# Optimization experiments

Measured on AMD Instinct MI355X. Metric: run time of the kernel, lower is better.

Reference implementation:

```python
import jax, jax.numpy as jnp
import numpy as np

N, C, E, H = 50000, 128, 1_600_000, 32
JITTER = 1e-20


def _lin(k, fan_in, fan_out):
    return jax.random.normal(k, (fan_in, fan_out), jnp.float32) / np.sqrt(fan_in)


def setup_inputs() -> dict:
    key = jax.random.key(0)
    ks = jax.random.split(key, 20)
    x = jax.random.normal(ks[0], (N, C), jnp.float32)
    edge_index = jax.random.randint(ks[1], (2, E), 0, N, dtype=jnp.int64)
    inp = {"x": x, "edge_index": edge_index}
    # actor params
    inp["aW"] = _lin(ks[2], C, C); inp["ab"] = jnp.zeros((C,), jnp.float32)
    inp["a1W"] = _lin(ks[3], C, H); inp["a1b"] = jnp.zeros((H,), jnp.float32)
    inp["a2W"] = _lin(ks[4], H, H); inp["a2b"] = jnp.zeros((H,), jnp.float32)
    inp["a3W"] = _lin(ks[5], H, 2); inp["a3b"] = jnp.zeros((2,), jnp.float32)
    # critic params
    inp["cW"] = _lin(ks[6], C, C); inp["cb"] = jnp.zeros((C,), jnp.float32)
    inp["c1W"] = _lin(ks[7], C, H); inp["c1b"] = jnp.zeros((H,), jnp.float32)
    inp["c2W"] = _lin(ks[8], H, H); inp["c2b"] = jnp.zeros((H,), jnp.float32)
    inp["c3W"] = _lin(ks[9], H, 2); inp["c3b"] = jnp.zeros((2,), jnp.float32)
    return inp


def gcn_conv(x, src, dst, W, b):
    """Standard PyG GCNConv: add self-loops, symmetric degree norm, X@W, scatter-add, +bias."""
    n = x.shape[0]
    loop = jnp.arange(n)
    s = jnp.concatenate([src, loop])  # [E+N]
    d = jnp.concatenate([dst, loop])
    deg = jax.ops.segment_sum(jnp.ones_like(d, jnp.float32), d, num_segments=n)
    dinv = jnp.where(deg > 0, jax.lax.rsqrt(deg), 0.0)
    norm = dinv[s] * dinv[d]                     # [E+N]
    h = x @ W                                    # [N, C]
    agg = jax.ops.segment_sum(h[s] * norm[:, None], d, num_segments=n)
    return agg + b


def reference(x, edge_index, aW, ab, a1W, a1b, a2W, a2b, a3W, a3b,
              cW, cb, c1W, c1b, c2W, c2b, c3W, c3b):
    src, dst = edge_index[0], edge_index[1]
    # actor
    h = jax.nn.relu(gcn_conv(x, src, dst, aW, ab)) + x
    h = jax.nn.relu(h @ a1W + a1b)
    h = jax.nn.relu(h @ a2W + a2b)
    a = h @ a3W + a3b                            # [N, 2]
    concentration = jax.nn.softplus(a[:, 0]) + JITTER
    p = jax.nn.softplus(a[:, 1])
    action2_probs = p / jnp.sum(p)
    # critic
    hc = jax.nn.relu(gcn_conv(x, src, dst, cW, cb)) + x
    hc = jnp.sum(hc, axis=0)                     # [C]
    hc = jax.nn.relu(hc @ c1W + c1b)
    hc = jax.nn.relu(hc @ c2W + c2b)
    value = hc @ c3W + c3b                       # [2]
    return (concentration, value, action2_probs)
```

## Files before the change

kernel.cpp:

```cpp
#include <hip/hip_runtime.h>
#include <hip/hip_bf16.h>
#include <hip/hip_fp16.h>
#include <math.h>

#define C 128
#define BCAP 12288

using half8x = __attribute__((ext_vector_type(8))) _Float16;
using half4x = __attribute__((ext_vector_type(4))) _Float16;
using f32x4  = __attribute__((ext_vector_type(4))) float;

__device__ inline float4 h4_to_f4(uint2 u) {
    __half2 p0 = *(__half2*)&u.x;
    __half2 p1 = *(__half2*)&u.y;
    float2 f0 = __half22float2(p0), f1 = __half22float2(p1);
    return make_float4(f0.x, f0.y, f1.x, f1.y);
}

__device__ inline float softplusf(float v) {
    return (v > 20.f) ? v : log1pf(expf(v));
}

__global__ __launch_bounds__(256) void initk(unsigned* gcur, float* colsum, float* pSum) {
    int t = threadIdx.x;
    gcur[t] = 0u;
    if (t < 128) colsum[t] = 0.f;
    if (t == 128) pSum[0] = 0.f;
}

__global__ __launch_bounds__(256) void wtk(const float* __restrict__ aW, const float* __restrict__ cW,
                                           const float* __restrict__ a1W,
                                           __half* __restrict__ wt, __half* __restrict__ a1wt) {
    int idx = blockIdx.x * 256 + threadIdx.x;
    if (idx < 32768) {
        int y = idx >> 14, r = idx & 16383;
        int k = r >> 7, n = r & 127;
        const float* W = y ? cW : aW;
        wt[((size_t)y << 14) + n * 128 + k] = __float2half(W[k * 128 + n]);
    } else if (idx < 36864) {
        int r = idx - 32768;
        int k = r >> 5, n = r & 31;
        a1wt[n * 128 + k] = __float2half(a1W[k * 32 + n]);
    }
}

__global__ __launch_bounds__(256) void bink(const int* __restrict__ ei,
                                            unsigned* __restrict__ gcur,
                                            unsigned* __restrict__ gstage,
                                            int E, int NBKT) {
    __shared__ unsigned raw[6400];
    __shared__ unsigned image[6400];
    __shared__ unsigned cnt[256];
    __shared__ unsigned pref[256];
    __shared__ unsigned cur[256];
    __shared__ unsigned gb[256];
    int t = threadIdx.x, b = blockIdx.x;
    int elo = (int)((long long)b * E / 256);
    int ehi = (int)((long long)(b + 1) * E / 256);
    int n = ehi - elo;

    for (int i = t; i < n; i += 256) {
        int d = __builtin_nontemporal_load(ei + E + elo + i);
        int s = __builtin_nontemporal_load(ei + elo + i);
        raw[i] = (unsigned)s | ((unsigned)(d & 255) << 16) | ((unsigned)(d >> 8) << 24);
    }
    cnt[t] = 0u; cur[t] = 0u;
    __syncthreads();
    for (int i = t; i < n; i += 256) atomicAdd(&cnt[raw[i] >> 24], 1u);
    __syncthreads();
    pref[t] = cnt[t];
    __syncthreads();
    for (int off = 1; off < 256; off <<= 1) {
        unsigned add = (t >= off) ? pref[t - off] : 0u;
        __syncthreads();
        pref[t] += add;
        __syncthreads();
    }
    gb[t] = (t < NBKT && cnt[t]) ? atomicAdd(&gcur[t], cnt[t]) : 0u;
    __syncthreads();
    for (int i = t; i < n; i += 256) {
        unsigned v = raw[i];
        unsigned B = v >> 24;
        unsigned pos = (pref[B] - cnt[B]) + atomicAdd(&cur[B], 1u);
        image[pos] = v & 0xFFFFFFu;
    }
    __syncthreads();
    int wv = t >> 6, lane = t & 63;
    for (int B = wv; B < NBKT; B += 4) {
        unsigned c = cnt[B];
        if (!c) continue;
        unsigned eb = pref[B] - c;
        unsigned gbase = gb[B];
        unsigned c2 = (gbase < BCAP) ? ((c < BCAP - gbase) ? c : BCAP - gbase) : 0u;
        for (unsigned i = lane; i < c2; i += 64)
            gstage[(size_t)B * BCAP + gbase + i] = image[eb + i];
    }
}

__global__ void bktscank(const unsigned* __restrict__ gcur, unsigned* __restrict__ bktbase, int NBKT) {
    __shared__ unsigned tmp[256];
    int t = threadIdx.x;
    unsigned g = (t < NBKT) ? gcur[t] : 0u;
    unsigned v = (g < BCAP) ? g : BCAP;
    tmp[t] = v;
    __syncthreads();
    for (int off = 1; off < 256; off <<= 1) {
        unsigned add = (t >= off) ? tmp[t - off] : 0u;
        __syncthreads();
        tmp[t] += add;
        __syncthreads();
    }
    if (t < NBKT) bktbase[t] = tmp[t] - v;
}

__global__ __launch_bounds__(256) void placek(const unsigned* __restrict__ gstage,
                                              const unsigned* __restrict__ gcur,
                                              const unsigned* __restrict__ bktbase,
                                              int* __restrict__ rowptr, float* __restrict__ dinv,
                                              int* __restrict__ col, int N, int NBKT) {
    __shared__ unsigned image[BCAP];
    __shared__ unsigned cnt[256];
    __shared__ unsigned pref[256];
    __shared__ unsigned cur[256];
    int B = blockIdx.x, t = threadIdx.x;
    unsigned g = gcur[B];
    unsigned m = (g < BCAP) ? g : BCAP;
    unsigned base = bktbase[B];
    const unsigned* st = gstage + (size_t)B * BCAP;

    cnt[t] = 0u; cur[t] = 0u;
    __syncthreads();
    for (unsigned i = t; i < m; i += 256) atomicAdd(&cnt[(st[i] >> 16) & 255u], 1u);
    __syncthreads();
    pref[t] = cnt[t];
    __syncthreads();
    for (int off = 1; off < 256; off <<= 1) {
        unsigned add = (t >= off) ? pref[t - off] : 0u;
        __syncthreads();
        pref[t] += add;
        __syncthreads();
    }
    int d = B * 256 + t;
    if (d < N) {
        rowptr[d] = (int)(base + pref[t] - cnt[t]);
        dinv[d] = rsqrtf((float)(cnt[t] + 1u));
    }
    if (B == NBKT - 1 && t == 0) rowptr[N] = (int)(base + m);
    for (unsigned i = t; i < m; i += 256) {
        unsigned v = st[i];
        unsigned dl = (v >> 16) & 255u;
        unsigned pos = (pref[dl] - cnt[dl]) + atomicAdd(&cur[dl], 1u);
        image[pos] = v & 0xFFFFu;
    }
    __syncthreads();
    for (unsigned i = t; i < m; i += 256) col[base + i] = (int)image[i];
}

__global__ __launch_bounds__(256) void xhk(const float* __restrict__ x, const float* __restrict__ dinv,
                                           __half* __restrict__ xh, __half* __restrict__ x16, int N) {
    int i = blockIdx.x * 256 + threadIdx.x;
    if (i >= N * 64) return;
    int node = i >> 6, fp = (i & 63) * 2;
    float w = dinv[node];
    float2 f = *(const float2*)&x[(size_t)node * C + fp];
    __half2 h = __floats2half2_rn(f.x * w, f.y * w);
    __half2 hx = __floats2half2_rn(f.x, f.y);
    *(unsigned*)&xh[(size_t)node * C + fp] = *(unsigned*)&h;
    *(unsigned*)&x16[(size_t)node * C + fp] = *(unsigned*)&hx;
}

__global__ __launch_bounds__(256) void gatherk(const int* __restrict__ col,
                                               const int* __restrict__ rowptr,
                                               const __half* __restrict__ xh,
                                               const float* __restrict__ dinv,
                                               __half* __restrict__ gg, int N) {
    __shared__ int snb[4][64];
    int t = threadIdx.x;
    int wid = t >> 6, lane = t & 63;
    int d = blockIdx.x * 4 + wid;
    if (d >= N) return;
    int beg = rowptr[d], end = rowptr[d + 1];
    int half = lane >> 5, sub = lane & 31;
    int f = sub * 4;

    float a0 = 0.f, a1 = 0.f, a2 = 0.f, a3 = 0.f;

    for (int c = beg; c < end; c += 64) {
        if (c + lane < end) snb[wid][lane] = col[c + lane];
        int n = end - c; if (n > 64) n = 64;
        int j = 0;
        for (; j + 3 < n; j += 4) {
            size_t i0 = (size_t)snb[wid][j + half] * C + f;
            size_t i1 = (size_t)snb[wid][j + 2 + half] * C + f;
            float4 v0 = h4_to_f4(*(const uint2*)&xh[i0]);
            float4 v1 = h4_to_f4(*(const uint2*)&xh[i1]);
            a0 += v0.x + v1.x;
            a1 += v0.y + v1.y;
            a2 += v0.z + v1.z;
            a3 += v0.w + v1.w;
        }
        for (; j < n; j += 2) {
            if (j + half < n) {
                float4 v = h4_to_f4(*(const uint2*)&xh[(size_t)snb[wid][j + half] * C + f]);
                a0 += v.x; a1 += v.y; a2 += v.z; a3 += v.w;
            }
        }
    }
    a0 += __shfl_xor(a0, 32, 64);
    a1 += __shfl_xor(a1, 32, 64);
    a2 += __shfl_xor(a2, 32, 64);
    a3 += __shfl_xor(a3, 32, 64);

    if (half == 0) {
        float4 s4 = h4_to_f4(*(const uint2*)&xh[(size_t)d * C + f]);
        float dv = dinv[d];
        __half2 h0 = __floats2half2_rn((a0 + s4.x) * dv, (a1 + s4.y) * dv);
        __half2 h1 = __floats2half2_rn((a2 + s4.z) * dv, (a3 + s4.w) * dv);
        uint2 u; u.x = *(unsigned*)&h0; u.y = *(unsigned*)&h1;
        *(uint2*)&gg[(size_t)d * C + f] = u;
    }
}

__global__ __launch_bounds__(256) void gemm2k(const __half* __restrict__ gg,
                                              const __half* __restrict__ wt,
                                              const __half* __restrict__ a1wt,
                                              const float* __restrict__ ab, const float* __restrict__ cb,
                                              const __half* __restrict__ x16,
                                              const float* __restrict__ a1b,
                                              const float* __restrict__ a2W, const float* __restrict__ a2b,
                                              const float* __restrict__ a3W, const float* __restrict__ a3b,
                                              float* __restrict__ scratch,
                                              float* __restrict__ out, float* __restrict__ pSum, int N) {
    __shared__ char As[16384];
    __shared__ char Aux[8192];
    const bool actor = (blockIdx.y == 0);
    const float* bias = actor ? ab : cb;
    const __half* W = wt + (actor ? 0 : 16384);
    const int row0 = blockIdx.x * 64;
    const int t = threadIdx.x;

    _Float16* w2t = (_Float16*)Aux;
    _Float16* h1b = (_Float16*)(Aux + 2560);
    float* w3s    = (float*)(Aux + 7680);
    float* scol   = (float*)Aux;

#pragma unroll
    for (int i = 0; i < 4; ++i) {
        int c = t + i * 256;
        int row = c >> 4, cb16 = (c & 15) * 16;
        int grow = row0 + row;
        uint4 u = make_uint4(0u, 0u, 0u, 0u);
        if (grow < N) u = *(const uint4*)&gg[(size_t)grow * C + (c & 15) * 8];
        *(uint4*)(As + row * 256 + (cb16 ^ ((row & 7) << 4))) = u;
    }
    if (actor) {
#pragma unroll
        for (int i = 0; i < 4; ++i) {
            int idx = t + i * 256;
            int k = idx >> 5, n = idx & 31;
            w2t[n * 40 + k] = (_Float16)a2W[idx];
        }
        if (t < 64) w3s[t] = a3W[t];
    }
    __syncthreads();

    int wv = t >> 6, l = t & 63;
    int lm = l & 15, lk = l >> 4;
    int koffB = lk * 16;
    int koffH = lk * 8;

    const int rowA = wv * 16 + lm;
    const int grow = row0 + rowA;
    const bool valid = grow < N;
    const int sw = (rowA & 7) << 4;

    half8x af[4];
    {
        const char* rp = As + rowA * 256;
#pragma unroll
        for (int kc = 0; kc < 4; ++kc)
            af[kc] = *(const half8x*)(rp + ((kc * 64 + koffB) ^ sw));
    }

#pragma unroll
    for (int nc = 0; nc < 8; ++nc) {
        const __half* wp = W + (nc * 16 + lm) * 128;
        half8x bf[4];
#pragma unroll
        for (int kc = 0; kc < 4; ++kc)
            bf[kc] = *(const half8x*)(wp + kc * 32 + koffH);
        f32x4 acc = {0.f, 0.f, 0.f, 0.f};
#pragma unroll
        for (int kc = 0; kc < 4; ++kc)
            acc = __builtin_amdgcn_mfma_f32_16x16x32_f16(bf[kc], af[kc], acc, 0, 0, 0);
        float4 bv = *(const float4*)&bias[nc * 16 + lk * 4];
        half4x xq = {};
        if (valid) xq = *(const half4x*)&x16[(size_t)grow * C + nc * 16 + lk * 4];
        float v0 = valid ? fmaxf(acc[0] + bv.x, 0.f) + (float)xq[0] : 0.f;
        float v1 = valid ? fmaxf(acc[1] + bv.y, 0.f) + (float)xq[1] : 0.f;
        float v2 = valid ? fmaxf(acc[2] + bv.z, 0.f) + (float)xq[2] : 0.f;
        float v3 = valid ? fmaxf(acc[3] + bv.w, 0.f) + (float)xq[3] : 0.f;
        if (actor) {
            half4x hv = { (_Float16)v0, (_Float16)v1, (_Float16)v2, (_Float16)v3 };
            *(half4x*)(As + rowA * 256 + ((nc * 32 + lk * 8) ^ sw)) = hv;
        } else {
            v0 += __shfl_xor(v0, 1, 64); v0 += __shfl_xor(v0, 2, 64);
            v0 += __shfl_xor(v0, 4, 64); v0 += __shfl_xor(v0, 8, 64);
            v1 += __shfl_xor(v1, 1, 64); v1 += __shfl_xor(v1, 2, 64);
            v1 += __shfl_xor(v1, 4, 64); v1 += __shfl_xor(v1, 8, 64);
            v2 += __shfl_xor(v2, 1, 64); v2 += __shfl_xor(v2, 2, 64);
            v2 += __shfl_xor(v2, 4, 64); v2 += __shfl_xor(v2, 8, 64);
            v3 += __shfl_xor(v3, 1, 64); v3 += __shfl_xor(v3, 2, 64);
            v3 += __shfl_xor(v3, 4, 64); v3 += __shfl_xor(v3, 8, 64);
            if (lm == 0) {
                float4 st = make_float4(v0, v1, v2, v3);
                *(float4*)&scol[wv * 128 + nc * 16 + lk * 4] = st;
            }
        }
    }
    __syncthreads();

    if (actor) {
        half8x a1f[4];
        {
            const char* rp = As + rowA * 256;
#pragma unroll
            for (int kc = 0; kc < 4; ++kc)
                a1f[kc] = *(const half8x*)(rp + ((kc * 64 + koffB) ^ sw));
        }
#pragma unroll
        for (int ct = 0; ct < 2; ++ct) {
            const __half* ap = a1wt + (ct * 16 + lm) * 128;
            f32x4 acc1 = {0.f, 0.f, 0.f, 0.f};
#pragma unroll
            for (int kc = 0; kc < 4; ++kc) {
                half8x bq = *(const half8x*)(ap + kc * 32 + koffH);
                acc1 = __builtin_amdgcn_mfma_f32_16x16x32_f16(bq, a1f[kc], acc1, 0, 0, 0);
            }
            float4 b1v = *(const float4*)&a1b[ct * 16 + lk * 4];
            half4x h = { (_Float16)fmaxf(acc1[0] + b1v.x, 0.f),
                         (_Float16)fmaxf(acc1[1] + b1v.y, 0.f),
                         (_Float16)fmaxf(acc1[2] + b1v.z, 0.f),
                         (_Float16)fmaxf(acc1[3] + b1v.w, 0.f) };
            *(half4x*)((char*)h1b + rowA * 80 + ct * 32 + lk * 8) = h;
        }

        half4x alo = *(const half4x*)((char*)h1b + rowA * 80 + lk * 16);
        half4x ahi = *(const half4x*)((char*)h1b + rowA * 80 + lk * 16 + 8);
        half8x a2f = __builtin_shufflevector(alo, ahi, 0, 1, 2, 3, 4, 5, 6, 7);
        float p0 = 0.f, p1 = 0.f;
#pragma unroll
        for (int ct = 0; ct < 2; ++ct) {
            half4x blo = *(const half4x*)((char*)w2t + (ct * 16 + lm) * 80 + lk * 16);
            half4x bhi = *(const half4x*)((char*)w2t + (ct * 16 + lm) * 80 + lk * 16 + 8);
            half8x b2f = __builtin_shufflevector(blo, bhi, 0, 1, 2, 3, 4, 5, 6, 7);
            f32x4 acc2 = {0.f, 0.f, 0.f, 0.f};
            acc2 = __builtin_amdgcn_mfma_f32_16x16x32_f16(b2f, a2f, acc2, 0, 0, 0);
            float4 b2v = *(const float4*)&a2b[ct * 16 + lk * 4];
#pragma unroll
            for (int j = 0; j < 4; ++j) {
                int f = ct * 16 + lk * 4 + j;
                float h2v = fmaxf(acc2[j] + (&b2v.x)[j], 0.f);
                float2 w3 = *(const float2*)&w3s[f * 2];
                p0 += h2v * w3.x;
                p1 += h2v * w3.y;
            }
        }
        p0 += __shfl_xor(p0, 16, 64); p0 += __shfl_xor(p0, 32, 64);
        p1 += __shfl_xor(p1, 16, 64); p1 += __shfl_xor(p1, 32, 64);
        float wave_psum = 0.f;
        if (lk == 0 && valid) {
            float s0 = softplusf(p0 + a3b[0]);
            float s1 = softplusf(p1 + a3b[1]);
            out[grow] = s0 + 1e-20f;
            out[(size_t)N + 2 + grow] = s1;
            wave_psum = s1;
        }
        wave_psum += __shfl_xor(wave_psum, 1, 64);
        wave_psum += __shfl_xor(wave_psum, 2, 64);
        wave_psum += __shfl_xor(wave_psum, 4, 64);
        wave_psum += __shfl_xor(wave_psum, 8, 64);
        wave_psum += __shfl_xor(wave_psum, 16, 64);
        wave_psum += __shfl_xor(wave_psum, 32, 64);
        if (l == 0) atomicAdd(pSum, wave_psum);
    } else {
        if (t < 128)
            scratch[(size_t)blockIdx.x * 128 + t] = scol[t] + scol[128 + t] + scol[256 + t] + scol[384 + t];
    }
}

__global__ __launch_bounds__(128) void csredk(const float* __restrict__ scratch, float* __restrict__ colsum, int nblk) {
    int t = threadIdx.x;
    float s = 0.f;
    for (int b = blockIdx.x; b < nblk; b += gridDim.x)
        s += scratch[(size_t)b * 128 + t];
    atomicAdd(&colsum[t], s);
}

__global__ void critick(const float* __restrict__ colsum,
                        const float* __restrict__ c1W, const float* __restrict__ c1b,
                        const float* __restrict__ c2W, const float* __restrict__ c2b,
                        const float* __restrict__ c3W, const float* __restrict__ c3b,
                        float* __restrict__ out, int N) {
    __shared__ float s1[32], s2[32];
    int t = threadIdx.x;
    if (t < 32) {
        float acc = c1b[t];
        for (int k = 0; k < 128; ++k) acc += colsum[k] * c1W[k * 32 + t];
        s1[t] = fmaxf(acc, 0.f);
    }
    __syncthreads();
    if (t < 32) {
        float acc = c2b[t];
        for (int k = 0; k < 32; ++k) acc += s1[k] * c2W[k * 32 + t];
        s2[t] = fmaxf(acc, 0.f);
    }
    __syncthreads();
    if (t < 2) {
        float acc = c3b[t];
        for (int k = 0; k < 32; ++k) acc += s2[k] * c3W[k * 2 + t];
        out[(size_t)N + t] = acc;
    }
}

__global__ __launch_bounds__(256) void normk(float* __restrict__ out, const float* __restrict__ pSum, int N) {
    int i = blockIdx.x * 256 + threadIdx.x;
    if (i < N) out[(size_t)N + 2 + i] /= pSum[0];
}

extern "C" void kernel_launch(void* const* d_in, const int* in_sizes, int n_in,
                              void* d_out, int out_size, void* d_ws, size_t ws_size,
                              hipStream_t stream) {
    const float* x   = (const float*)d_in[0];
    const int* ei    = (const int*)d_in[1];
    const float* aW  = (const float*)d_in[2];
    const float* ab  = (const float*)d_in[3];
    const float* a1W = (const float*)d_in[4];
    const float* a1b = (const float*)d_in[5];
    const float* a2W = (const float*)d_in[6];
    const float* a2b = (const float*)d_in[7];
    const float* a3W = (const float*)d_in[8];
    const float* a3b = (const float*)d_in[9];
    const float* cW  = (const float*)d_in[10];
    const float* cb  = (const float*)d_in[11];
    const float* c1W = (const float*)d_in[12];
    const float* c1b = (const float*)d_in[13];
    const float* c2W = (const float*)d_in[14];
    const float* c2b = (const float*)d_in[15];
    const float* c3W = (const float*)d_in[16];
    const float* c3b = (const float*)d_in[17];

    const int N = in_sizes[0] / C;
    const int E = in_sizes[1] / 2;
    const int NBKT = (N + 255) / 256;
    const int nblk64 = (N + 63) / 64;
    float* out = (float*)d_out;

    char* ws = (char*)d_ws;
    size_t off = 0;
    auto alloc = [&](size_t bytes) {
        size_t o = off;
        off = (off + bytes + 255) & ~(size_t)255;
        return (void*)(ws + o);
    };
    unsigned* gcur    = (unsigned*)alloc(256 * 4);
    unsigned* bktbase = (unsigned*)alloc(256 * 4);
    unsigned* gstage  = (unsigned*)alloc((size_t)NBKT * BCAP * 4);
    int* rowptr       = (int*)alloc((size_t)(N + 1) * 4);
    float* dinv       = (float*)alloc((size_t)N * 4);
    int* colidx       = (int*)alloc((size_t)E * 4);
    __half* xh        = (__half*)alloc((size_t)N * C * 2);
    __half* x16       = (__half*)alloc((size_t)N * C * 2);
    __half* gg        = (__half*)alloc((size_t)N * C * 2);
    __half* wt        = (__half*)alloc(2 * 16384 * 2);
    __half* a1wt      = (__half*)alloc(4096 * 2);
    float* scratch    = (float*)alloc((size_t)nblk64 * 128 * 4);
    float* colsum     = (float*)alloc(128 * 4);
    float* pSum       = (float*)alloc(4);

    initk<<<1, 256, 0, stream>>>(gcur, colsum, pSum);
    wtk<<<144, 256, 0, stream>>>(aW, cW, a1W, wt, a1wt);
    bink<<<256, 256, 0, stream>>>(ei, gcur, gstage, E, NBKT);
    bktscank<<<1, 256, 0, stream>>>(gcur, bktbase, NBKT);
    placek<<<NBKT, 256, 0, stream>>>(gstage, gcur, bktbase, rowptr, dinv, colidx, N, NBKT);
    xhk<<<(N * 64 + 255) / 256, 256, 0, stream>>>(x, dinv, xh, x16, N);
    gatherk<<<(N + 3) / 4, 256, 0, stream>>>(colidx, rowptr, xh, dinv, gg, N);
    gemm2k<<<dim3(nblk64, 2), 256, 0, stream>>>(gg, wt, a1wt, ab, cb, x16,
                                                a1b, a2W, a2b, a3W, a3b,
                                                scratch, out, pSum, N);
    csredk<<<8, 128, 0, stream>>>(scratch, colsum, nblk64);
    critick<<<1, 64, 0, stream>>>(colsum, c1W, c1b, c2W, c2b, c3W, c3b, out, N);
    normk<<<(N + 255) / 256, 256, 0, stream>>>(out, pSum, N);
}
```

Measured before the change: 236.5 us.

## Merge actor and critic GEMM blocks into one block sharing the A tile

Before, separate blocks handled the actor and the critic, and each one loaded the same 64-row aggregated feature tile and the same x16 residual. Now one block per row tile runs both 128x128 MFMA GEMMs from a single A-fragment load, then does the critic column reduction and the actor MLP head. Weight fragments for the next column chunk are prefetched into registers while the current one computes. This halves the gg and x16 reads and the block count, but raises register pressure (two accumulator and weight sets plus prefetch buffers) and LDS use, which may lower occupancy.

```diff
diff --git a/kernel.cpp b/kernel.cpp
--- a/kernel.cpp
+++ b/kernel.cpp
@@ -232,17 +232,14 @@
                                               float* __restrict__ scratch,
                                               float* __restrict__ out, float* __restrict__ pSum, int N) {
     __shared__ char As[16384];
-    __shared__ char Aux[8192];
-    const bool actor = (blockIdx.y == 0);
-    const float* bias = actor ? ab : cb;
-    const __half* W = wt + (actor ? 0 : 16384);
-    const int row0 = blockIdx.x * 64;
-    const int t = threadIdx.x;
-
+    __shared__ char Aux[10240];
     _Float16* w2t = (_Float16*)Aux;
     _Float16* h1b = (_Float16*)(Aux + 2560);
     float* w3s    = (float*)(Aux + 7680);
-    float* scol   = (float*)Aux;
+    float* scol   = (float*)(Aux + 7936);
+
+    const int row0 = blockIdx.x * 64;
+    const int t = threadIdx.x;
 
 #pragma unroll
     for (int i = 0; i < 4; ++i) {
@@ -253,15 +250,13 @@
         if (grow < N) u = *(const uint4*)&gg[(size_t)grow * C + (c & 15) * 8];
         *(uint4*)(As + row * 256 + (cb16 ^ ((row & 7) << 4))) = u;
     }
-    if (actor) {
-#pragma unroll
-        for (int i = 0; i < 4; ++i) {
-            int idx = t + i * 256;
-            int k = idx >> 5, n = idx & 31;
-            w2t[n * 40 + k] = (_Float16)a2W[idx];
-        }
-        if (t < 64) w3s[t] = a3W[t];
-    }
+#pragma unroll
+    for (int i = 0; i < 4; ++i) {
+        int idx = t + i * 256;
+        int k = idx >> 5, n = idx & 31;
+        w2t[n * 40 + k] = (_Float16)a2W[idx];
+    }
+    if (t < 64) w3s[t] = a3W[t];
     __syncthreads();
 
     int wv = t >> 6, l = t & 63;
@@ -282,28 +277,55 @@
             af[kc] = *(const half8x*)(rp + ((kc * 64 + koffB) ^ sw));
     }
 
+    const __half* WA = wt;
+    const __half* WC = wt + 16384;
+
+    half8x bfA[4], bfC[4];
+    {
+        const __half* wpA = WA + lm * 128;
+        const __half* wpC = WC + lm * 128;
+#pragma unroll
+        for (int kc = 0; kc < 4; ++kc) {
+            bfA[kc] = *(const half8x*)(wpA + kc * 32 + koffH);
+            bfC[kc] = *(const half8x*)(wpC + kc * 32 + koffH);
+        }
+    }
+
 #pragma unroll
     for (int nc = 0; nc < 8; ++nc) {
-        const __half* wp = W + (nc * 16 + lm) * 128;
-        half8x bf[4];
-#pragma unroll
-        for (int kc = 0; kc < 4; ++kc)
-            bf[kc] = *(const half8x*)(wp + kc * 32 + koffH);
-        f32x4 acc = {0.f, 0.f, 0.f, 0.f};
-#pragma unroll
-        for (int kc = 0; kc < 4; ++kc)
-            acc = __builtin_amdgcn_mfma_f32_16x16x32_f16(bf[kc], af[kc], acc, 0, 0, 0);
-        float4 bv = *(const float4*)&bias[nc * 16 + lk * 4];
+        half8x nA[4], nC[4];
+        if (nc < 7) {
+            const __half* wpA = WA + ((nc + 1) * 16 + lm) * 128;
+            const __half* wpC = WC + ((nc + 1) * 16 + lm) * 128;
+#pragma unroll
+            for (int kc = 0; kc < 4; ++kc) {
+                nA[kc] = *(const half8x*)(wpA + kc * 32 + koffH);
+                nC[kc] = *(const half8x*)(wpC + kc * 32 + koffH);
+            }
+        }
+        f32x4 accA = {0.f, 0.f, 0.f, 0.f};
+        f32x4 accC = {0.f, 0.f, 0.f, 0.f};
+#pragma unroll
+        for (int kc = 0; kc < 4; ++kc) {
+            accA = __builtin_amdgcn_mfma_f32_16x16x32_f16(bfA[kc], af[kc], accA, 0, 0, 0);
+            accC = __builtin_amdgcn_mfma_f32_16x16x32_f16(bfC[kc], af[kc], accC, 0, 0, 0);
+        }
+        float4 bvA = *(const float4*)&ab[nc * 16 + lk * 4];
+        float4 bvC = *(const float4*)&cb[nc * 16 + lk * 4];
         half4x xq = {};
         if (valid) xq = *(const half4x*)&x16[(size_t)grow * C + nc * 16 + lk * 4];
-        float v0 = valid ? fmaxf(acc[0] + bv.x, 0.f) + (float)xq[0] : 0.f;
-        float v1 = valid ? fmaxf(acc[1] + bv.y, 0.f) + (float)xq[1] : 0.f;
-        float v2 = valid ? fmaxf(acc[2] + bv.z, 0.f) + (float)xq[2] : 0.f;
-        float v3 = valid ? fmaxf(acc[3] + bv.w, 0.f) + (float)xq[3] : 0.f;
-        if (actor) {
-            half4x hv = { (_Float16)v0, (_Float16)v1, (_Float16)v2, (_Float16)v3 };
+        {
+            half4x hv = { (_Float16)(valid ? fmaxf(accA[0] + bvA.x, 0.f) + (float)xq[0] : 0.f),
+                          (_Float16)(valid ? fmaxf(accA[1] + bvA.y, 0.f) + (float)xq[1] : 0.f),
+                          (_Float16)(valid ? fmaxf(accA[2] + bvA.z, 0.f) + (float)xq[2] : 0.f),
+                          (_Float16)(valid ? fmaxf(accA[3] + bvA.w, 0.f) + (float)xq[3] : 0.f) };
             *(half4x*)(As + rowA * 256 + ((nc * 32 + lk * 8) ^ sw)) = hv;
-        } else {
+        }
+        {
+            float v0 = valid ? fmaxf(accC[0] + bvC.x, 0.f) + (float)xq[0] : 0.f;
+            float v1 = valid ? fmaxf(accC[1] + bvC.y, 0.f) + (float)xq[1] : 0.f;
+            float v2 = valid ? fmaxf(accC[2] + bvC.z, 0.f) + (float)xq[2] : 0.f;
+            float v3 = valid ? fmaxf(accC[3] + bvC.w, 0.f) + (float)xq[3] : 0.f;
             v0 += __shfl_xor(v0, 1, 64); v0 += __shfl_xor(v0, 2, 64);
             v0 += __shfl_xor(v0, 4, 64); v0 += __shfl_xor(v0, 8, 64);
             v1 += __shfl_xor(v1, 1, 64); v1 += __shfl_xor(v1, 2, 64);
@@ -312,81 +334,81 @@
             v2 += __shfl_xor(v2, 4, 64); v2 += __shfl_xor(v2, 8, 64);
             v3 += __shfl_xor(v3, 1, 64); v3 += __shfl_xor(v3, 2, 64);
             v3 += __shfl_xor(v3, 4, 64); v3 += __shfl_xor(v3, 8, 64);
-            if (lm == 0) {
-                float4 st = make_float4(v0, v1, v2, v3);
-                *(float4*)&scol[wv * 128 + nc * 16 + lk * 4] = st;
-            }
-        }
-    }
-    __syncthreads();
-
-    if (actor) {
-        half8x a1f[4];
-        {
-            const char* rp = As + rowA * 256;
-#pragma unroll
-            for (int kc = 0; kc < 4; ++kc)
-                a1f[kc] = *(const half8x*)(rp + ((kc * 64 + koffB) ^ sw));
-        }
-#pragma unroll
-        for (int ct = 0; ct < 2; ++ct) {
-            const __half* ap = a1wt + (ct * 16 + lm) * 128;
-            f32x4 acc1 = {0.f, 0.f, 0.f, 0.f};
-#pragma unroll
-            for (int kc = 0; kc < 4; ++kc) {
-                half8x bq = *(const half8x*)(ap + kc * 32 + koffH);
-                acc1 = __builtin_amdgcn_mfma_f32_16x16x32_f16(bq, a1f[kc], acc1, 0, 0, 0);
-            }
-            float4 b1v = *(const float4*)&a1b[ct * 16 + lk * 4];
-            half4x h = { (_Float16)fmaxf(acc1[0] + b1v.x, 0.f),
-                         (_Float16)fmaxf(acc1[1] + b1v.y, 0.f),
-                         (_Float16)fmaxf(acc1[2] + b1v.z, 0.f),
-                         (_Float16)fmaxf(acc1[3] + b1v.w, 0.f) };
-            *(half4x*)((char*)h1b + rowA * 80 + ct * 32 + lk * 8) = h;
-        }
-
-        half4x alo = *(const half4x*)((char*)h1b + rowA * 80 + lk * 16);
-        half4x ahi = *(const half4x*)((char*)h1b + rowA * 80 + lk * 16 + 8);
-        half8x a2f = __builtin_shufflevector(alo, ahi, 0, 1, 2, 3, 4, 5, 6, 7);
-        float p0 = 0.f, p1 = 0.f;
-#pragma unroll
-        for (int ct = 0; ct < 2; ++ct) {
-            half4x blo = *(const half4x*)((char*)w2t + (ct * 16 + lm) * 80 + lk * 16);
-            half4x bhi = *(const half4x*)((char*)w2t + (ct * 16 + lm) * 80 + lk * 16 + 8);
-            half8x b2f = __builtin_shufflevector(blo, bhi, 0, 1, 2, 3, 4, 5, 6, 7);
-            f32x4 acc2 = {0.f, 0.f, 0.f, 0.f};
-            acc2 = __builtin_amdgcn_mfma_f32_16x16x32_f16(b2f, a2f, acc2, 0, 0, 0);
-            float4 b2v = *(const float4*)&a2b[ct * 16 + lk * 4];
-#pragma unroll
-            for (int j = 0; j < 4; ++j) {
-                int f = ct * 16 + lk * 4 + j;
-                float h2v = fmaxf(acc2[j] + (&b2v.x)[j], 0.f);
-                float2 w3 = *(const float2*)&w3s[f * 2];
-                p0 += h2v * w3.x;
-                p1 += h2v * w3.y;
-            }
-        }
-        p0 += __shfl_xor(p0, 16, 64); p0 += __shfl_xor(p0, 32, 64);
-        p1 += __shfl_xor(p1, 16, 64); p1 += __shfl_xor(p1, 32, 64);
-        float wave_psum = 0.f;
-        if (lk == 0 && valid) {
-            float s0 = softplusf(p0 + a3b[0]);
-            float s1 = softplusf(p1 + a3b[1]);
-            out[grow] = s0 + 1e-20f;
-            out[(size_t)N + 2 + grow] = s1;
-            wave_psum = s1;
-        }
-        wave_psum += __shfl_xor(wave_psum, 1, 64);
-        wave_psum += __shfl_xor(wave_psum, 2, 64);
-        wave_psum += __shfl_xor(wave_psum, 4, 64);
-        wave_psum += __shfl_xor(wave_psum, 8, 64);
-        wave_psum += __shfl_xor(wave_psum, 16, 64);
-        wave_psum += __shfl_xor(wave_psum, 32, 64);
-        if (l == 0) atomicAdd(pSum, wave_psum);
-    } else {
-        if (t < 128)
-            scratch[(size_t)blockIdx.x * 128 + t] = scol[t] + scol[128 + t] + scol[256 + t] + scol[384 + t];
-    }
+            if (lm == 0)
+                *(float4*)&scol[wv * 128 + nc * 16 + lk * 4] = make_float4(v0, v1, v2, v3);
+        }
+        if (nc < 7) {
+#pragma unroll
+            for (int kc = 0; kc < 4; ++kc) { bfA[kc] = nA[kc]; bfC[kc] = nC[kc]; }
+        }
+    }
+    __syncthreads();
+
+    if (t < 128)
+        scratch[(size_t)blockIdx.x * 128 + t] = scol[t] + scol[128 + t] + scol[256 + t] + scol[384 + t];
+
+    half8x a1f[4];
+    {
+        const char* rp = As + rowA * 256;
+#pragma unroll
+        for (int kc = 0; kc < 4; ++kc)
+            a1f[kc] = *(const half8x*)(rp + ((kc * 64 + koffB) ^ sw));
+    }
+#pragma unroll
+    for (int ct = 0; ct < 2; ++ct) {
+        const __half* ap = a1wt + (ct * 16 + lm) * 128;
+        f32x4 acc1 = {0.f, 0.f, 0.f, 0.f};
+#pragma unroll
+        for (int kc = 0; kc < 4; ++kc) {
+            half8x bq = *(const half8x*)(ap + kc * 32 + koffH);
+            acc1 = __builtin_amdgcn_mfma_f32_16x16x32_f16(bq, a1f[kc], acc1, 0, 0, 0);
+        }
+        float4 b1v = *(const float4*)&a1b[ct * 16 + lk * 4];
+        half4x h = { (_Float16)fmaxf(acc1[0] + b1v.x, 0.f),
+                     (_Float16)fmaxf(acc1[1] + b1v.y, 0.f),
+                     (_Float16)fmaxf(acc1[2] + b1v.z, 0.f),
+                     (_Float16)fmaxf(acc1[3] + b1v.w, 0.f) };
+        *(half4x*)((char*)h1b + rowA * 80 + ct * 32 + lk * 8) = h;
+    }
+
+    half4x alo = *(const half4x*)((char*)h1b + rowA * 80 + lk * 16);
+    half4x ahi = *(const half4x*)((char*)h1b + rowA * 80 + lk * 16 + 8);
+    half8x a2f = __builtin_shufflevector(alo, ahi, 0, 1, 2, 3, 4, 5, 6, 7);
+    float p0 = 0.f, p1 = 0.f;
+#pragma unroll
+    for (int ct = 0; ct < 2; ++ct) {
+        half4x blo = *(const half4x*)((char*)w2t + (ct * 16 + lm) * 80 + lk * 16);
+        half4x bhi = *(const half4x*)((char*)w2t + (ct * 16 + lm) * 80 + lk * 16 + 8);
+        half8x b2f = __builtin_shufflevector(blo, bhi, 0, 1, 2, 3, 4, 5, 6, 7);
+        f32x4 acc2 = {0.f, 0.f, 0.f, 0.f};
+        acc2 = __builtin_amdgcn_mfma_f32_16x16x32_f16(b2f, a2f, acc2, 0, 0, 0);
+        float4 b2v = *(const float4*)&a2b[ct * 16 + lk * 4];
+#pragma unroll
+        for (int j = 0; j < 4; ++j) {
+            int f = ct * 16 + lk * 4 + j;
+            float h2v = fmaxf(acc2[j] + (&b2v.x)[j], 0.f);
+            float2 w3 = *(const float2*)&w3s[f * 2];
+            p0 += h2v * w3.x;
+            p1 += h2v * w3.y;
+        }
+    }
+    p0 += __shfl_xor(p0, 16, 64); p0 += __shfl_xor(p0, 32, 64);
+    p1 += __shfl_xor(p1, 16, 64); p1 += __shfl_xor(p1, 32, 64);
+    float wave_psum = 0.f;
+    if (lk == 0 && valid) {
+        float s0 = softplusf(p0 + a3b[0]);
+        float s1 = softplusf(p1 + a3b[1]);
+        out[grow] = s0 + 1e-20f;
+        out[(size_t)N + 2 + grow] = s1;
+        wave_psum = s1;
+    }
+    wave_psum += __shfl_xor(wave_psum, 1, 64);
+    wave_psum += __shfl_xor(wave_psum, 2, 64);
+    wave_psum += __shfl_xor(wave_psum, 4, 64);
+    wave_psum += __shfl_xor(wave_psum, 8, 64);
+    wave_psum += __shfl_xor(wave_psum, 16, 64);
+    wave_psum += __shfl_xor(wave_psum, 32, 64);
+    if (l == 0) atomicAdd(pSum, wave_psum);
 }
 
 __global__ __launch_bounds__(128) void csredk(const float* __restrict__ scratch, float* __restrict__ colsum, int nblk) {
@@ -485,9 +507,9 @@
     placek<<<NBKT, 256, 0, stream>>>(gstage, gcur, bktbase, rowptr, dinv, colidx, N, NBKT);
     xhk<<<(N * 64 + 255) / 256, 256, 0, stream>>>(x, dinv, xh, x16, N);
     gatherk<<<(N + 3) / 4, 256, 0, stream>>>(colidx, rowptr, xh, dinv, gg, N);
-    gemm2k<<<dim3(nblk64, 2), 256, 0, stream>>>(gg, wt, a1wt, ab, cb, x16,
-                                                a1b, a2W, a2b, a3W, a3b,
-                                                scratch, out, pSum, N);
+    gemm2k<<<nblk64, 256, 0, stream>>>(gg, wt, a1wt, ab, cb, x16,
+                                       a1b, a2W, a2b, a3W, a3b,
+                                       scratch, out, pSum, N);
     csredk<<<8, 128, 0, stream>>>(scratch, colsum, nblk64);
     critick<<<1, 64, 0, stream>>>(colsum, c1W, c1b, c2W, c2b, c3W, c3b, out, N);
     normk<<<(N + 255) / 256, 256, 0, stream>>>(out, pSum, N);
```

Result: faster. 228.1 us (-3.5%).
